# Kernel tuning notes

Measured on AMD Instinct MI355X. Metric: run time of the kernel, lower is better.

## Reference

```python
import jax, jax.numpy as jnp
import numpy as np

B, N, T = 512, 128, 64
ALPHA = 0.5  # LeakyReLU negative slope
NEG = jnp.float32(-9e15)


def _gat(h, mask, W, a):
    # GraphAttentionLayer with concat=True (trailing relu), eval mode (no dropout)
    Wh = h @ W                                   # [B,N,F]
    F = W.shape[1]
    e1 = Wh @ a[:F]                              # [B,N,1]
    e2 = Wh @ a[F:]                              # [B,N,1]
    e = jax.nn.leaky_relu(e1 + jnp.swapaxes(e2, 1, 2), ALPHA)  # [B,N,N]
    e = jnp.where(mask, e, NEG)
    att = jax.nn.softmax(e, axis=1)              # torch softmax dim=1 (over rows)
    return jax.nn.relu(jnp.matmul(att, Wh))


def _lstm_layer(x, wih, whh, bih, bhh):
    # x: [T,B,in]; hidden size 1; torch gate order i,f,g,o
    h0 = jnp.zeros((x.shape[1], 1), x.dtype)
    def step(carry, xt):
        h, c = carry
        g = xt @ wih.T + h @ whh.T + bih + bhh   # [B,4]
        i, f, gg, o = jnp.split(g, 4, axis=-1)
        c = jax.nn.sigmoid(f) * c + jax.nn.sigmoid(i) * jnp.tanh(gg)
        h = jax.nn.sigmoid(o) * jnp.tanh(c)
        return (h, c), h
    _, ys = jax.lax.scan(step, (h0, h0), x)
    return ys                                    # [T,B,1]


def setup_inputs() -> dict:
    key = jax.random.key(0)
    ks = jax.random.split(key, 32)
    def xu(k, shape, gain=1.414):
        lim = gain * np.sqrt(6.0 / (shape[0] + shape[1]))
        return jax.random.uniform(k, shape, jnp.float32, -lim, lim)
    d = {}
    d["adjacency"] = jax.random.randint(ks[0], (B, N, N), 0, 2, dtype=jnp.int32)
    d["feature"] = jax.random.normal(ks[1], (B, N), jnp.float32)
    d["time"] = jax.random.normal(ks[2], (B, N), jnp.float32)
    d["interval_popularity"] = jax.random.normal(ks[3], (B, T), jnp.float32)
    # GAT params
    d["W1"] = xu(ks[4], (1, 512)); d["a1"] = xu(ks[5], (1024, 1))
    d["W2"] = xu(ks[6], (512, 8)); d["a2"] = xu(ks[7], (16, 1))
    # attention-pooling params (torch.randn in original)
    d["Weight"] = jax.random.normal(ks[8], (128, 128), jnp.float32)
    d["Wv"] = jax.random.normal(ks[9], (128, 128), jnp.float32)
    # 2-layer LSTM(1->1)
    d["wih0"] = jax.random.normal(ks[10], (4, 1)) * 0.5
    d["whh0"] = jax.random.normal(ks[11], (4, 1)) * 0.5
    d["bih0"] = jax.random.normal(ks[12], (4,)) * 0.5
    d["bhh0"] = jax.random.normal(ks[13], (4,)) * 0.5
    d["wih1"] = jax.random.normal(ks[14], (4, 1)) * 0.5
    d["whh1"] = jax.random.normal(ks[15], (4, 1)) * 0.5
    d["bih1"] = jax.random.normal(ks[16], (4,)) * 0.5
    d["bhh1"] = jax.random.normal(ks[17], (4,)) * 0.5
    # MultiheadAttention(embed_dim=1, heads=1)
    d["mha_in_w"] = jax.random.normal(ks[18], (3, 1)) * 0.5
    d["mha_in_b"] = jnp.zeros((3,), jnp.float32)
    d["mha_out_w"] = jax.random.normal(ks[19], (1, 1)) * 0.5
    d["mha_out_b"] = jnp.zeros((1,), jnp.float32)
    # FL MLP: 192->128->32->1 (stored as [in,out])
    d["fl1_w"] = xu(ks[20], (192, 128), 1.0); d["fl1_b"] = jnp.zeros((128,), jnp.float32)
    d["fl2_w"] = xu(ks[21], (128, 32), 1.0);  d["fl2_b"] = jnp.zeros((32,), jnp.float32)
    d["fl3_w"] = xu(ks[22], (32, 1), 1.0);    d["fl3_b"] = jnp.zeros((1,), jnp.float32)
    return d


def reference(adjacency, feature, time, interval_popularity,
              W1, a1, W2, a2, Weight, Wv,
              wih0, whh0, bih0, bhh0, wih1, whh1, bih1, bhh1,
              mha_in_w, mha_in_b, mha_out_w, mha_out_b,
              fl1_w, fl1_b, fl2_w, fl2_b, fl3_w, fl3_b):
    mask = adjacency > 0
    x = feature.reshape(B, N, -1)                # [B,128,1]
    h = _gat(x, mask, W1, a1)                    # [B,128,512]
    h = jax.nn.relu(h)
    h = _gat(h, mask, W2, a2)                    # [B,128,8]

    xs = jnp.swapaxes(interval_popularity.reshape(B, -1, 1), 0, 1)  # [T,B,1]
    xs = _lstm_layer(xs, wih0, whh0, bih0, bhh0)
    xs = _lstm_layer(xs, wih1, whh1, bih1, bhh1)
    ip = jnp.swapaxes(xs, 0, 1).reshape(B, -1)   # [B,64]

    h = jnp.mean(h, axis=2, keepdims=True)       # [B,128,1]
    Wt = time.reshape(B, N, -1)                  # [B,128,1]
    att = jnp.concatenate([h, Wt], axis=2)       # [B,128,2]
    att = jnp.swapaxes(jnp.swapaxes(att, 1, 2) @ Weight, 1, 2)  # [B,128,2]
    att = jax.nn.softmax(att, axis=2)
    hv = jnp.swapaxes(jnp.concatenate([h, Wt], axis=2), 1, 2)   # [B,2,128]
    hv = jax.nn.relu((hv @ Wv).reshape(B, N, -1))  # faithful reshape (not transpose)
    h = jnp.sum(hv * att, axis=2)                # [B,128]

    h = jnp.concatenate([h, ip], axis=1)         # [B,192]
    hq = h[..., None]                            # [B,192,1]
    q = hq * mha_in_w[0, 0] + mha_in_b[0]
    k = hq * mha_in_w[1, 0] + mha_in_b[1]
    v = hq * mha_in_w[2, 0] + mha_in_b[2]
    a = jax.nn.softmax(q @ jnp.swapaxes(k, 1, 2), axis=-1)  # scale=1/sqrt(1)
    ho = (a @ v) * mha_out_w[0, 0] + mha_out_b[0]
    h = (ho + hq).reshape(B, -1)                 # [B,192]

    h = jax.nn.relu(h @ fl1_w + fl1_b)
    h = jnp.tanh(h @ fl2_w + fl2_b)
    h = jax.nn.relu(h @ fl3_w + fl3_b)           # [B,1]
    return h
```

## Files before the change

kernel.cpp:

```cpp
#include <hip/hip_runtime.h>
#include <math.h>

typedef unsigned int uint;
typedef unsigned long long ull;

#define L2E 1.44269504f

__device__ __forceinline__ float lrelu(float z){ return fmaxf(z, 0.5f*z); }
__device__ __forceinline__ float reluf(float z){ return fmaxf(z, 0.f); }
__device__ __forceinline__ float fexp(float z){ return __builtin_amdgcn_exp2f(z*L2E); }
__device__ __forceinline__ float frcp(float z){ return __builtin_amdgcn_rcpf(z); }
__device__ __forceinline__ float tanh_n(float z){
  return __fmaf_rn(2.f, __builtin_amdgcn_rcpf(1.f + __builtin_amdgcn_exp2f(-2.f*L2E*z)), -1.f);
}

__global__ __launch_bounds__(512, 4) void fused_kernel(
    const int* __restrict__ adj, const float* __restrict__ feat,
    const float* __restrict__ timei,
    const float* __restrict__ Weight, const float* __restrict__ Wv,
    const float* __restrict__ W1, const float* __restrict__ a1,
    const float* __restrict__ W2, const float* __restrict__ a2,
    const float* __restrict__ ipop,
    const float* __restrict__ wih0, const float* __restrict__ whh0,
    const float* __restrict__ bih0, const float* __restrict__ bhh0,
    const float* __restrict__ wih1, const float* __restrict__ whh1,
    const float* __restrict__ bih1, const float* __restrict__ bhh1,
    const float* __restrict__ mha_in_w, const float* __restrict__ mha_in_b,
    const float* __restrict__ mha_out_w, const float* __restrict__ mha_out_b,
    const float* __restrict__ fl1_w, const float* __restrict__ fl1_b,
    const float* __restrict__ fl2_w, const float* __restrict__ fl2_b,
    const float* __restrict__ fl3_w, const float* __restrict__ fl3_b,
    float* __restrict__ out)
{
  const int b = blockIdx.x, t = threadIdx.x;
  const int lane = t & 127, h = t >> 7;
  const int wv = t >> 6, ln = t & 63;

  __shared__ ull   rowW[256];
  __shared__ float xs[128], tim[128], hm[128], eAs[128], rho_s[128];
  __shared__ float2 f2a[128];
  __shared__ float  red1[4][128];
  __shared__ float2 red4[4][128];
  __shared__ float4 q4[128];
  __shared__ float4 pool4[4][128];
  __shared__ float2 kv[192];
  __shared__ float  hq[192], h2s[192];
  __shared__ float  pden[2][192], pnum[2][192];
  __shared__ float  sred[8];
  __shared__ float  cpart[8][2];
  __shared__ float  pqpart[8][16];
  __shared__ float  cons[24];
  __shared__ float  ips[64];

  if (t < 128){ xs[t] = feat[b*128 + t]; tim[t] = timei[b*128 + t]; }

  float a2reg[16];
  if (t == 0){
    #pragma unroll
    for (int g = 0; g < 16; ++g) a2reg[g] = a2[g];
  }

  float h1v=0.f, c1s=0.f, h2v=0.f, c2s=0.f;
  float wi0s[4], wh0s[4], bb0s[4], wi1s[4], wh1s[4], bb1s[4];
  const float4* xsrc4 = (const float4*)(ipop + b*64);
  float4 xcur0, xcur1;
  if (t == 511){
    #pragma unroll
    for (int k = 0; k < 4; ++k){
      const float s = (k == 2) ? -2.f*L2E : -L2E;
      wi0s[k]=wih0[k]*s; wh0s[k]=whh0[k]*s; bb0s[k]=(bih0[k]+bhh0[k])*s;
      wi1s[k]=wih1[k]*s; wh1s[k]=whh1[k]*s; bb1s[k]=(bih1[k]+bhh1[k])*s;
    }
    xcur0 = xsrc4[0]; xcur1 = xsrc4[1];
  }
  auto lstm8 = [&](int c){
    if (t != 511) return;
    const float4 xa = xcur0, xb = xcur1;
    if (c < 7){ xcur0 = xsrc4[2*c+2]; xcur1 = xsrc4[2*c+3]; }
    float o[8];
    #pragma unroll
    for (int si = 0; si < 8; ++si){
      const float x = (si==0)?xa.x:(si==1)?xa.y:(si==2)?xa.z:(si==3)?xa.w:
                      (si==4)?xb.x:(si==5)?xb.y:(si==6)?xb.z:xb.w;
      float gi = frcp(1.f + __builtin_amdgcn_exp2f(__fmaf_rn(x, wi0s[0], __fmaf_rn(h1v, wh0s[0], bb0s[0]))));
      float gf = frcp(1.f + __builtin_amdgcn_exp2f(__fmaf_rn(x, wi0s[1], __fmaf_rn(h1v, wh0s[1], bb0s[1]))));
      float gg = __fmaf_rn(2.f, frcp(1.f + __builtin_amdgcn_exp2f(__fmaf_rn(x, wi0s[2], __fmaf_rn(h1v, wh0s[2], bb0s[2])))), -1.f);
      float go = frcp(1.f + __builtin_amdgcn_exp2f(__fmaf_rn(x, wi0s[3], __fmaf_rn(h1v, wh0s[3], bb0s[3]))));
      c1s = gf*c1s + gi*gg;  h1v = go*tanh_n(c1s);
      float hi = frcp(1.f + __builtin_amdgcn_exp2f(__fmaf_rn(h1v, wi1s[0], __fmaf_rn(h2v, wh1s[0], bb1s[0]))));
      float hf = frcp(1.f + __builtin_amdgcn_exp2f(__fmaf_rn(h1v, wi1s[1], __fmaf_rn(h2v, wh1s[1], bb1s[1]))));
      float hg = __fmaf_rn(2.f, frcp(1.f + __builtin_amdgcn_exp2f(__fmaf_rn(h1v, wi1s[2], __fmaf_rn(h2v, wh1s[2], bb1s[2])))), -1.f);
      float ho = frcp(1.f + __builtin_amdgcn_exp2f(__fmaf_rn(h1v, wi1s[3], __fmaf_rn(h2v, wh1s[3], bb1s[3])))) ;
      c2s = hf*c2s + hi*hg;  h2v = ho*tanh_n(c2s);
      o[si] = h2v;
    }
    #pragma unroll
    for (int si = 0; si < 8; ++si) ips[8*c + si] = o[si];
  };

  {
    const int* abase = adj + (((long)b) << 14) + wv*2048 + ln;
    ull myword = 0;
    #pragma unroll
    for (int blk = 0; blk < 4; ++blk){
      int v[8];
      #pragma unroll
      for (int q = 0; q < 8; ++q) v[q] = abase[(blk*8 + q)*64];
      #pragma unroll
      for (int q = 0; q < 8; ++q){
        ull m = __ballot(v[q] > 0);
        myword = (ln == blk*8 + q) ? m : myword;
      }
    }
    if (ln < 32) rowW[wv*32 + ln] = myword;
  }

  {
    float w0 = W1[t];
    float s1 = w0*a1[t];
    float s2 = w0*a1[512+t];
    #pragma unroll
    for (int off = 32; off; off >>= 1){ s1 += __shfl_xor(s1, off); s2 += __shfl_xor(s2, off); }
    if (ln == 0){ cpart[wv][0] = s1; cpart[wv][1] = s2; }
  }
  {
    const float w = W1[t];
    const float wp = fmaxf(w, 0.f), wn = fminf(w, 0.f);
    const float4 A = *(const float4*)(W2 + t*8);
    const float4 Bv = *(const float4*)(W2 + t*8 + 4);
    float accP[8], accQ[8];
    accP[0]=wp*A.x;  accQ[0]=wn*A.x;   accP[1]=wp*A.y;  accQ[1]=wn*A.y;
    accP[2]=wp*A.z;  accQ[2]=wn*A.z;   accP[3]=wp*A.w;  accQ[3]=wn*A.w;
    accP[4]=wp*Bv.x; accQ[4]=wn*Bv.x;  accP[5]=wp*Bv.y; accQ[5]=wn*Bv.y;
    accP[6]=wp*Bv.z; accQ[6]=wn*Bv.z;  accP[7]=wp*Bv.w; accQ[7]=wn*Bv.w;
    #pragma unroll
    for (int g = 0; g < 8; ++g){
      float p = accP[g], q = accQ[g];
      #pragma unroll
      for (int off = 32; off; off >>= 1){ p += __shfl_xor(p, off); q += __shfl_xor(q, off); }
      if (ln == 0){ pqpart[wv][g] = p; pqpart[wv][8+g] = q; }
    }
  }
  __syncthreads();

  const uint rowm = (uint)(rowW[lane*2 + (h>>1)] >> ((h&1)*32));
  uint colm = 0;
  {
    const int wsel = lane >> 6, bsel = lane & 63;
    #pragma unroll
    for (int k = 0; k < 32; ++k)
      colm |= (uint)((rowW[(32*h + k)*2 + wsel] >> bsel) & 1ull) << k;
  }
  if (t < 64){
    float mx = fmaxf(xs[t], xs[t+64]);
    float mn = fminf(xs[t], xs[t+64]);
    #pragma unroll
    for (int off = 32; off; off >>= 1){
      mx = fmaxf(mx, __shfl_xor(mx, off));
      mn = fminf(mn, __shfl_xor(mn, off));
    }
    if (t == 0){ sred[0] = mx; sred[1] = mn; }
  }
  if (t == 0){
    float c1v = 0.f, c2v = 0.f;
    #pragma unroll
    for (int wvi = 0; wvi < 8; ++wvi){ c1v += cpart[wvi][0]; c2v += cpart[wvi][1]; }
    cons[0] = c1v; cons[1] = c2v;
    float pAx=0.f, qAx=0.f, pBx=0.f, qBx=0.f;
    #pragma unroll
    for (int g = 0; g < 8; ++g){
      float P = 0.f, Q = 0.f;
      #pragma unroll
      for (int wvi = 0; wvi < 8; ++wvi){ P += pqpart[wvi][g]; Q += pqpart[wvi][8+g]; }
      cons[2+g] = P; cons[10+g] = Q;
      pAx = __fmaf_rn(P, a2reg[g],   pAx);  qAx = __fmaf_rn(Q, a2reg[g],   qAx);
      pBx = __fmaf_rn(P, a2reg[8+g], pBx);  qBx = __fmaf_rn(Q, a2reg[8+g], qBx);
    }
    cons[18]=pAx; cons[19]=qAx; cons[20]=pBx; cons[21]=qBx;
  }
  lstm8(0);
  __syncthreads();

  float myE1=0.f, myRho=0.f, myx=0.f;
  {
    const float c1 = cons[0], c2 = cons[1];
    const float rmax = (c1 >= 0.f) ? c1*sred[0] : c1*sred[1];
    if (t < 128){
      myx = xs[t];
      float r  = c1*myx;
      float cj = c2*myx;
      float d  = r - rmax;
      myE1 = fexp(d);
      float Eh = fexp(0.5f*d);
      myRho = fexp(-0.5f*fmaxf(rmax + cj, -170.f));
      f2a[t] = make_float2(myE1, Eh);
      rho_s[t] = myRho;
    }
  }
  lstm8(1);
  __syncthreads();

  {
    const float rho = rho_s[lane];
    float s = 0.f;
    #pragma unroll
    for (int k = 0; k < 32; ++k){
      float2 E = f2a[32*h + k];
      float v = fmaxf(E.x, rho*E.y);
      s += ((colm >> k) & 1u) ? v : 0.f;
    }
    red1[h][lane] = s;
  }
  lstm8(2);
  __syncthreads();

  if (t < 128){
    float s = red1[0][t] + red1[1][t] + red1[2][t] + red1[3][t];
    float sinv = frcp(s);
    float ax = fabsf(myx)*sinv;
    q4[t] = make_float4(ax, myRho*ax, (myx >= 0.f) ? 1.f : -1.f, 0.f);
  }
  lstm8(3);
  __syncthreads();

  {
    const float om = frcp(f2a[lane].y);
    float acc = 0.f;
    #pragma unroll
    for (int k = 0; k < 32; ++k){
      float4 G = q4[32*h + k];
      float v = fmaxf(G.x, om*G.y);
      float sg = ((rowm >> k) & 1u) ? G.z : 0.f;
      acc = __fmaf_rn(v, sg, acc);
    }
    red1[h][lane] = acc;
  }
  lstm8(4);
  __syncthreads();

  float u = 0.f, eBv = 0.f, eAv = 0.f;
  if (t < 128){
    u = myE1*(red1[0][t] + red1[1][t] + red1[2][t] + red1[3][t]);
    eAv = (u >= 0.f ? cons[18] : cons[19])*u;
    eBv = (u >= 0.f ? cons[20] : cons[21])*u;
    eAs[t] = eAv;
  }
  lstm8(5);
  __syncthreads();

  if (t < 64){
    float mx = fmaxf(eAs[t], eAs[t+64]);
    #pragma unroll
    for (int off = 32; off; off >>= 1) mx = fmaxf(mx, __shfl_xor(mx, off));
    if (t == 0) sred[2] = mx;
  }
  lstm8(6);
  __syncthreads();

  float myE1b=0.f;
  {
    const float eAmax = sred[2];
    if (t < 128){
      float d2 = eAv - eAmax;
      myE1b = fexp(d2);
      float Ehb = fexp(0.5f*d2);
      float rho2 = fexp(-0.5f*fmaxf(eAmax + eBv, -170.f));
      f2a[t] = make_float2(myE1b, Ehb);
      rho_s[t] = rho2;
    }
  }
  lstm8(7);
  __syncthreads();

  {
    const float rho = rho_s[lane];
    float s = 0.f;
    #pragma unroll
    for (int k = 0; k < 32; ++k){
      float2 E = f2a[32*h + k];
      float v = fmaxf(E.x, rho*E.y);
      s += ((colm >> k) & 1u) ? v : 0.f;
    }
    red1[h][lane] = s;
  }
  __syncthreads();

  if (t < 128){
    float s = red1[0][t] + red1[1][t] + red1[2][t] + red1[3][t];
    float sinv = frcp(s);
    float rho2 = rho_s[t];
    float up = fmaxf(u, 0.f)*sinv, un = -fminf(u, 0.f)*sinv;
    q4[t] = make_float4(up, rho2*up, un, rho2*un);
  }
  __syncthreads();

  {
    const float om = frcp(f2a[lane].y);
    float accp = 0.f, accn = 0.f;
    #pragma unroll
    for (int k = 0; k < 32; ++k){
      float4 G = q4[32*h + k];
      bool m = ((rowm >> k) & 1u);
      float v1 = fmaxf(G.x, om*G.y);
      float v2 = fmaxf(G.z, om*G.w);
      accp += m ? v1 : 0.f;
      accn += m ? v2 : 0.f;
    }
    red4[h][lane] = make_float2(accp, accn);
  }
  __syncthreads();

  if (t < 128){
    float ap=0.f, an=0.f;
    #pragma unroll
    for (int g = 0; g < 4; ++g){ float2 v = red4[g][t]; ap += v.x; an += v.y; }
    float sp = myE1b*ap, sn = -myE1b*an;
    float acc = 0.f;
    #pragma unroll
    for (int g = 0; g < 8; ++g) acc += reluf(__fmaf_rn(sp, cons[2+g], sn*cons[10+g]));
    hm[t] = 0.125f*acc;
  }
  __syncthreads();

  {
    const int n = lane;
    float a0=0.f, a1v=0.f, v0=0.f, v1=0.f;
    const int m0 = h*32;
    #pragma unroll 8
    for (int k = 0; k < 32; ++k){
      int m = m0 + k;
      float hmv = hm[m], tv = tim[m];
      float wg = Weight[(m<<7) + n], wvv = Wv[(m<<7) + n];
      a0 = __fmaf_rn(hmv, wg, a0); a1v = __fmaf_rn(tv, wg, a1v);
      v0 = __fmaf_rn(hmv, wvv, v0); v1 = __fmaf_rn(tv, wvv, v1);
    }
    pool4[h][n] = make_float4(a0, a1v, v0, v1);
  }
  __syncthreads();

  float att0 = 0.f, att1 = 0.f, rsv = 0.f;
  if (t < 128){
    float A0=0.f, A1=0.f, V0=0.f, V1=0.f;
    #pragma unroll
    for (int g = 0; g < 4; ++g){ float4 v = pool4[g][t]; A0+=v.x; A1+=v.y; V0+=v.z; V1+=v.w; }
    red4[0][t] = make_float2(V0, V1);
    float mx = fmaxf(A0, A1);
    att0 = fexp(A0 - mx); att1 = fexp(A1 - mx);
    rsv = frcp(att0 + att1);
  }
  __syncthreads();

  if (t < 128){
    float r0, r1;
    if (t < 64){ r0 = red4[0][2*t].x;     r1 = red4[0][2*t+1].x; }
    else       { r0 = red4[0][2*t-128].y; r1 = red4[0][2*t-127].y; }
    hq[t] = (reluf(r0)*att0 + reluf(r1)*att1)*rsv;
  }
  if (t >= 192 && t < 256) hq[128 + (t - 192)] = ips[t - 192];
  __syncthreads();

  const float wq = mha_in_w[0], wk = mha_in_w[1], wvv_ = mha_in_w[2];
  const float bq = mha_in_b[0], bk = mha_in_b[1], bv = mha_in_b[2];
  const float wo = mha_out_w[0], bo = mha_out_b[0];
  if (t < 192){
    float hv_ = hq[t];
    kv[t] = make_float2(__fmaf_rn(hv_, wk, bk), __fmaf_rn(hv_, wvv_, bv));
  }
  __syncthreads();

  if (t < 64){
    float k0 = kv[t].x, k1 = kv[t+64].x, k2 = kv[t+128].x;
    float mx = fmaxf(fmaxf(k0, k1), k2);
    float mn = fminf(fminf(k0, k1), k2);
    #pragma unroll
    for (int off = 32; off; off >>= 1){
      mx = fmaxf(mx, __shfl_xor(mx, off));
      mn = fminf(mn, __shfl_xor(mn, off));
    }
    if (t == 0){ sred[3] = mx; sred[4] = mn; }
  }
  __syncthreads();

  if (t < 384){
    const int half = (t >= 192), tt = t - half*192;
    float qi = __fmaf_rn(hq[tt], wq, bq);
    float mx = (qi >= 0.f) ? qi*sred[3] : qi*sred[4];
    const float qi2 = qi*L2E, mx2 = mx*L2E;
    float den = 0.f, num = 0.f;
    const int j0 = half*96;
    #pragma unroll 8
    for (int jj = 0; jj < 96; ++jj){
      float2 K = kv[j0 + jj];
      float e = __builtin_amdgcn_exp2f(__fmaf_rn(qi2, K.x, -mx2));
      den += e; num = __fmaf_rn(e, K.y, num);
    }
    pden[half][tt] = den; pnum[half][tt] = num;
  }
  __syncthreads();

  if (t < 192){
    float den = pden[0][t] + pden[1][t];
    float num = pnum[0][t] + pnum[1][t];
    h2s[t] = __fmaf_rn(num*frcp(den), wo, bo) + hq[t];
  }
  __syncthreads();

  {
    const int n = t & 127, qtr = t >> 7;
    float acc = 0.f;
    const int i0 = qtr*48;
    #pragma unroll 8
    for (int k = 0; k < 48; ++k){
      int i = i0 + k;
      acc = __fmaf_rn(h2s[i], fl1_w[i*128 + n], acc);
    }
    red4[qtr][n].x = acc;
  }
  __syncthreads();

  if (t < 128) rho_s[t] = reluf(red4[0][t].x + red4[1][t].x + red4[2][t].x + red4[3][t].x + fl1_b[t]);
  __syncthreads();

  if (t < 128){
    const int n = t & 31, seg = t >> 5;
    float p = 0.f;
    #pragma unroll 8
    for (int k = 0; k < 32; ++k){
      int i = seg*32 + k;
      p = __fmaf_rn(rho_s[i], fl2_w[i*32 + n], p);
    }
    eAs[t] = p;
  }
  __syncthreads();

  if (t < 32) hm[t] = tanh_n(eAs[t] + eAs[t+32] + eAs[t+64] + eAs[t+96] + fl2_b[t]);
  __syncthreads();

  if (t < 64){
    float p = (t < 32) ? hm[t]*fl3_w[t] : 0.f;
    #pragma unroll
    for (int off = 32; off; off >>= 1) p += __shfl_xor(p, off);
    if (t == 0) out[b] = reluf(p + fl3_b[0]);
  }
}

extern "C" void kernel_launch(void* const* d_in, const int* in_sizes, int n_in,
                              void* d_out, int out_size, void* d_ws, size_t ws_size,
                              hipStream_t stream) {
  const int*   adj    = (const int*)  d_in[0];
  const float* feat   = (const float*)d_in[1];
  const float* timei  = (const float*)d_in[2];
  const float* ipop   = (const float*)d_in[3];
  const float* W1     = (const float*)d_in[4];
  const float* a1     = (const float*)d_in[5];
  const float* W2     = (const float*)d_in[6];
  const float* a2     = (const float*)d_in[7];
  const float* Weight = (const float*)d_in[8];
  const float* Wv     = (const float*)d_in[9];
  const float* wih0   = (const float*)d_in[10];
  const float* whh0   = (const float*)d_in[11];
  const float* bih0   = (const float*)d_in[12];
  const float* bhh0   = (const float*)d_in[13];
  const float* wih1   = (const float*)d_in[14];
  const float* whh1   = (const float*)d_in[15];
  const float* bih1   = (const float*)d_in[16];
  const float* bhh1   = (const float*)d_in[17];
  const float* mha_in_w  = (const float*)d_in[18];
  const float* mha_in_b  = (const float*)d_in[19];
  const float* mha_out_w = (const float*)d_in[20];
  const float* mha_out_b = (const float*)d_in[21];
  const float* fl1_w = (const float*)d_in[22];
  const float* fl1_b = (const float*)d_in[23];
  const float* fl2_w = (const float*)d_in[24];
  const float* fl2_b = (const float*)d_in[25];
  const float* fl3_w = (const float*)d_in[26];
  const float* fl3_b = (const float*)d_in[27];

  fused_kernel<<<512, 512, 0, stream>>>(adj, feat, timei, Weight, Wv,
                                        W1, a1, W2, a2, ipop,
                                        wih0, whh0, bih0, bhh0,
                                        wih1, whh1, bih1, bhh1,
                                        mha_in_w, mha_in_b, mha_out_w, mha_out_b,
                                        fl1_w, fl1_b, fl2_w, fl2_b, fl3_w, fl3_b,
                                        (float*)d_out);
}
```

Baseline: 49.29 us.

## Double block size to 1024 threads and halve per-thread work in every stage

Each block now runs 1024 threads instead of 512, and every stage is re-split so each thread does half as many items: adjacency ballots, GAT column sums, pooling, MHA key ranges and the FC layers. Reduction buffers grow to 8 partial slots. The goal is to cut the serial per-thread loop length and add wavefronts for latency hiding, given only 512 blocks. The cost is more partial-sum reduction, more register pressure under the tighter launch bound, and more threads sitting idle in the narrow stages.

```diff
diff --git a/kernel.cpp b/kernel.cpp
--- a/kernel.cpp
+++ b/kernel.cpp
@@ -6,7 +6,6 @@
 
 #define L2E 1.44269504f
 
-__device__ __forceinline__ float lrelu(float z){ return fmaxf(z, 0.5f*z); }
 __device__ __forceinline__ float reluf(float z){ return fmaxf(z, 0.f); }
 __device__ __forceinline__ float fexp(float z){ return __builtin_amdgcn_exp2f(z*L2E); }
 __device__ __forceinline__ float frcp(float z){ return __builtin_amdgcn_rcpf(z); }
@@ -14,7 +13,7 @@
   return __fmaf_rn(2.f, __builtin_amdgcn_rcpf(1.f + __builtin_amdgcn_exp2f(-2.f*L2E*z)), -1.f);
 }
 
-__global__ __launch_bounds__(512, 4) void fused_kernel(
+__global__ __launch_bounds__(1024, 8) void fused_kernel(
     const int* __restrict__ adj, const float* __restrict__ feat,
     const float* __restrict__ timei,
     const float* __restrict__ Weight, const float* __restrict__ Wv,
@@ -39,13 +38,13 @@
   __shared__ ull   rowW[256];
   __shared__ float xs[128], tim[128], hm[128], eAs[128], rho_s[128];
   __shared__ float2 f2a[128];
-  __shared__ float  red1[4][128];
-  __shared__ float2 red4[4][128];
+  __shared__ float  red1[8][128];
+  __shared__ float2 red2f[8][128];
   __shared__ float4 q4[128];
-  __shared__ float4 pool4[4][128];
+  __shared__ float4 pool4[8][128];
   __shared__ float2 kv[192];
   __shared__ float  hq[192], h2s[192];
-  __shared__ float  pden[2][192], pnum[2][192];
+  __shared__ float  pden[4][192], pnum[4][192];
   __shared__ float  sred[8];
   __shared__ float  cpart[8][2];
   __shared__ float  pqpart[8][16];
@@ -64,7 +63,7 @@
   float wi0s[4], wh0s[4], bb0s[4], wi1s[4], wh1s[4], bb1s[4];
   const float4* xsrc4 = (const float4*)(ipop + b*64);
   float4 xcur0, xcur1;
-  if (t == 511){
+  if (t == 1023){
     #pragma unroll
     for (int k = 0; k < 4; ++k){
       const float s = (k == 2) ? -2.f*L2E : -L2E;
@@ -74,7 +73,7 @@
     xcur0 = xsrc4[0]; xcur1 = xsrc4[1];
   }
   auto lstm8 = [&](int c){
-    if (t != 511) return;
+    if (t != 1023) return;
     const float4 xa = xcur0, xb = xcur1;
     if (c < 7){ xcur0 = xsrc4[2*c+2]; xcur1 = xsrc4[2*c+3]; }
     float o[8];
@@ -99,10 +98,10 @@
   };
 
   {
-    const int* abase = adj + (((long)b) << 14) + wv*2048 + ln;
+    const int* abase = adj + (((long)b) << 14) + wv*1024 + ln;
     ull myword = 0;
     #pragma unroll
-    for (int blk = 0; blk < 4; ++blk){
+    for (int blk = 0; blk < 2; ++blk){
       int v[8];
       #pragma unroll
       for (int q = 0; q < 8; ++q) v[q] = abase[(blk*8 + q)*64];
@@ -112,19 +111,17 @@
         myword = (ln == blk*8 + q) ? m : myword;
       }
     }
-    if (ln < 32) rowW[wv*32 + ln] = myword;
-  }
-
-  {
+    if (ln < 16) rowW[wv*16 + ln] = myword;
+  }
+
+  if (t < 512){
     float w0 = W1[t];
     float s1 = w0*a1[t];
     float s2 = w0*a1[512+t];
     #pragma unroll
     for (int off = 32; off; off >>= 1){ s1 += __shfl_xor(s1, off); s2 += __shfl_xor(s2, off); }
     if (ln == 0){ cpart[wv][0] = s1; cpart[wv][1] = s2; }
-  }
-  {
-    const float w = W1[t];
+    const float w = w0;
     const float wp = fmaxf(w, 0.f), wn = fminf(w, 0.f);
     const float4 A = *(const float4*)(W2 + t*8);
     const float4 Bv = *(const float4*)(W2 + t*8 + 4);
@@ -143,13 +140,13 @@
   }
   __syncthreads();
 
-  const uint rowm = (uint)(rowW[lane*2 + (h>>1)] >> ((h&1)*32));
+  const uint rowm = (uint)((rowW[lane*2 + (h>>2)] >> ((h&3)*16)) & 0xFFFFull);
   uint colm = 0;
   {
     const int wsel = lane >> 6, bsel = lane & 63;
-    #pragma unroll
-    for (int k = 0; k < 32; ++k)
-      colm |= (uint)((rowW[(32*h + k)*2 + wsel] >> bsel) & 1ull) << k;
+    #pragma unroll 8
+    for (int k = 0; k < 16; ++k)
+      colm |= (uint)((rowW[(16*h + k)*2 + wsel] >> bsel) & 1ull) << k;
   }
   if (t < 64){
     float mx = fmaxf(xs[t], xs[t+64]);
@@ -203,9 +200,9 @@
   {
     const float rho = rho_s[lane];
     float s = 0.f;
-    #pragma unroll
-    for (int k = 0; k < 32; ++k){
-      float2 E = f2a[32*h + k];
+    #pragma unroll 8
+    for (int k = 0; k < 16; ++k){
+      float2 E = f2a[16*h + k];
       float v = fmaxf(E.x, rho*E.y);
       s += ((colm >> k) & 1u) ? v : 0.f;
     }
@@ -215,7 +212,9 @@
   __syncthreads();
 
   if (t < 128){
-    float s = red1[0][t] + red1[1][t] + red1[2][t] + red1[3][t];
+    float s = 0.f;
+    #pragma unroll
+    for (int g = 0; g < 8; ++g) s += red1[g][t];
     float sinv = frcp(s);
     float ax = fabsf(myx)*sinv;
     q4[t] = make_float4(ax, myRho*ax, (myx >= 0.f) ? 1.f : -1.f, 0.f);
@@ -226,9 +225,9 @@
   {
     const float om = frcp(f2a[lane].y);
     float acc = 0.f;
-    #pragma unroll
-    for (int k = 0; k < 32; ++k){
-      float4 G = q4[32*h + k];
+    #pragma unroll 8
+    for (int k = 0; k < 16; ++k){
+      float4 G = q4[16*h + k];
       float v = fmaxf(G.x, om*G.y);
       float sg = ((rowm >> k) & 1u) ? G.z : 0.f;
       acc = __fmaf_rn(v, sg, acc);
@@ -240,7 +239,10 @@
 
   float u = 0.f, eBv = 0.f, eAv = 0.f;
   if (t < 128){
-    u = myE1*(red1[0][t] + red1[1][t] + red1[2][t] + red1[3][t]);
+    float s = 0.f;
+    #pragma unroll
+    for (int g = 0; g < 8; ++g) s += red1[g][t];
+    u = myE1*s;
     eAv = (u >= 0.f ? cons[18] : cons[19])*u;
     eBv = (u >= 0.f ? cons[20] : cons[21])*u;
     eAs[t] = eAv;
@@ -275,9 +277,9 @@
   {
     const float rho = rho_s[lane];
     float s = 0.f;
-    #pragma unroll
-    for (int k = 0; k < 32; ++k){
-      float2 E = f2a[32*h + k];
+    #pragma unroll 8
+    for (int k = 0; k < 16; ++k){
+      float2 E = f2a[16*h + k];
       float v = fmaxf(E.x, rho*E.y);
       s += ((colm >> k) & 1u) ? v : 0.f;
     }
@@ -286,7 +288,9 @@
   __syncthreads();
 
   if (t < 128){
-    float s = red1[0][t] + red1[1][t] + red1[2][t] + red1[3][t];
+    float s = 0.f;
+    #pragma unroll
+    for (int g = 0; g < 8; ++g) s += red1[g][t];
     float sinv = frcp(s);
     float rho2 = rho_s[t];
     float up = fmaxf(u, 0.f)*sinv, un = -fminf(u, 0.f)*sinv;
@@ -297,23 +301,23 @@
   {
     const float om = frcp(f2a[lane].y);
     float accp = 0.f, accn = 0.f;
-    #pragma unroll
-    for (int k = 0; k < 32; ++k){
-      float4 G = q4[32*h + k];
+    #pragma unroll 8
+    for (int k = 0; k < 16; ++k){
+      float4 G = q4[16*h + k];
       bool m = ((rowm >> k) & 1u);
       float v1 = fmaxf(G.x, om*G.y);
       float v2 = fmaxf(G.z, om*G.w);
       accp += m ? v1 : 0.f;
       accn += m ? v2 : 0.f;
     }
-    red4[h][lane] = make_float2(accp, accn);
+    red2f[h][lane] = make_float2(accp, accn);
   }
   __syncthreads();
 
   if (t < 128){
     float ap=0.f, an=0.f;
     #pragma unroll
-    for (int g = 0; g < 4; ++g){ float2 v = red4[g][t]; ap += v.x; an += v.y; }
+    for (int g = 0; g < 8; ++g){ float2 v = red2f[g][t]; ap += v.x; an += v.y; }
     float sp = myE1b*ap, sn = -myE1b*an;
     float acc = 0.f;
     #pragma unroll
@@ -325,9 +329,9 @@
   {
     const int n = lane;
     float a0=0.f, a1v=0.f, v0=0.f, v1=0.f;
-    const int m0 = h*32;
-    #pragma unroll 8
-    for (int k = 0; k < 32; ++k){
+    const int m0 = h*16;
+    #pragma unroll 8
+    for (int k = 0; k < 16; ++k){
       int m = m0 + k;
       float hmv = hm[m], tv = tim[m];
       float wg = Weight[(m<<7) + n], wvv = Wv[(m<<7) + n];
@@ -342,8 +346,8 @@
   if (t < 128){
     float A0=0.f, A1=0.f, V0=0.f, V1=0.f;
     #pragma unroll
-    for (int g = 0; g < 4; ++g){ float4 v = pool4[g][t]; A0+=v.x; A1+=v.y; V0+=v.z; V1+=v.w; }
-    red4[0][t] = make_float2(V0, V1);
+    for (int g = 0; g < 8; ++g){ float4 v = pool4[g][t]; A0+=v.x; A1+=v.y; V0+=v.z; V1+=v.w; }
+    red2f[0][t] = make_float2(V0, V1);
     float mx = fmaxf(A0, A1);
     att0 = fexp(A0 - mx); att1 = fexp(A1 - mx);
     rsv = frcp(att0 + att1);
@@ -352,8 +356,8 @@
 
   if (t < 128){
     float r0, r1;
-    if (t < 64){ r0 = red4[0][2*t].x;     r1 = red4[0][2*t+1].x; }
-    else       { r0 = red4[0][2*t-128].y; r1 = red4[0][2*t-127].y; }
+    if (t < 64){ r0 = red2f[0][2*t].x;     r1 = red2f[0][2*t+1].x; }
+    else       { r0 = red2f[0][2*t-128].y; r1 = red2f[0][2*t-127].y; }
     hq[t] = (reluf(r0)*att0 + reluf(r1)*att1)*rsv;
   }
   if (t >= 192 && t < 256) hq[128 + (t - 192)] = ips[t - 192];
@@ -381,59 +385,69 @@
   }
   __syncthreads();
 
-  if (t < 384){
-    const int half = (t >= 192), tt = t - half*192;
+  if (t < 768){
+    const int qtr = t / 192, tt = t - qtr*192;
     float qi = __fmaf_rn(hq[tt], wq, bq);
     float mx = (qi >= 0.f) ? qi*sred[3] : qi*sred[4];
     const float qi2 = qi*L2E, mx2 = mx*L2E;
     float den = 0.f, num = 0.f;
-    const int j0 = half*96;
-    #pragma unroll 8
-    for (int jj = 0; jj < 96; ++jj){
+    const int j0 = qtr*48;
+    #pragma unroll 8
+    for (int jj = 0; jj < 48; ++jj){
       float2 K = kv[j0 + jj];
       float e = __builtin_amdgcn_exp2f(__fmaf_rn(qi2, K.x, -mx2));
       den += e; num = __fmaf_rn(e, K.y, num);
     }
-    pden[half][tt] = den; pnum[half][tt] = num;
+    pden[qtr][tt] = den; pnum[qtr][tt] = num;
   }
   __syncthreads();
 
   if (t < 192){
-    float den = pden[0][t] + pden[1][t];
-    float num = pnum[0][t] + pnum[1][t];
+    float den = pden[0][t] + pden[1][t] + pden[2][t] + pden[3][t];
+    float num = pnum[0][t] + pnum[1][t] + pnum[2][t] + pnum[3][t];
     h2s[t] = __fmaf_rn(num*frcp(den), wo, bo) + hq[t];
   }
   __syncthreads();
 
   {
-    const int n = t & 127, qtr = t >> 7;
+    const int n = t & 127, oct = t >> 7;
     float acc = 0.f;
-    const int i0 = qtr*48;
-    #pragma unroll 8
-    for (int k = 0; k < 48; ++k){
+    const int i0 = oct*24;
+    #pragma unroll 8
+    for (int k = 0; k < 24; ++k){
       int i = i0 + k;
       acc = __fmaf_rn(h2s[i], fl1_w[i*128 + n], acc);
     }
-    red4[qtr][n].x = acc;
-  }
-  __syncthreads();
-
-  if (t < 128) rho_s[t] = reluf(red4[0][t].x + red4[1][t].x + red4[2][t].x + red4[3][t].x + fl1_b[t]);
-  __syncthreads();
-
-  if (t < 128){
+    red1[oct][n] = acc;
+  }
+  __syncthreads();
+
+  if (t < 128){
+    float s = fl1_b[t];
+    #pragma unroll
+    for (int g = 0; g < 8; ++g) s += red1[g][t];
+    rho_s[t] = reluf(s);
+  }
+  __syncthreads();
+
+  if (t < 256){
     const int n = t & 31, seg = t >> 5;
     float p = 0.f;
     #pragma unroll 8
-    for (int k = 0; k < 32; ++k){
-      int i = seg*32 + k;
+    for (int k = 0; k < 16; ++k){
+      int i = seg*16 + k;
       p = __fmaf_rn(rho_s[i], fl2_w[i*32 + n], p);
     }
-    eAs[t] = p;
-  }
-  __syncthreads();
-
-  if (t < 32) hm[t] = tanh_n(eAs[t] + eAs[t+32] + eAs[t+64] + eAs[t+96] + fl2_b[t]);
+    red1[seg][n] = p;
+  }
+  __syncthreads();
+
+  if (t < 32){
+    float s = fl2_b[t];
+    #pragma unroll
+    for (int g = 0; g < 8; ++g) s += red1[g][t];
+    hm[t] = tanh_n(s);
+  }
   __syncthreads();
 
   if (t < 64){
@@ -476,11 +490,11 @@
   const float* fl3_w = (const float*)d_in[26];
   const float* fl3_b = (const float*)d_in[27];
 
-  fused_kernel<<<512, 512, 0, stream>>>(adj, feat, timei, Weight, Wv,
-                                        W1, a1, W2, a2, ipop,
-                                        wih0, whh0, bih0, bhh0,
-                                        wih1, whh1, bih1, bhh1,
-                                        mha_in_w, mha_in_b, mha_out_w, mha_out_b,
-                                        fl1_w, fl1_b, fl2_w, fl2_b, fl3_w, fl3_b,
-                                        (float*)d_out);
+  fused_kernel<<<512, 1024, 0, stream>>>(adj, feat, timei, Weight, Wv,
+                                         W1, a1, W2, a2, ipop,
+                                         wih0, whh0, bih0, bhh0,
+                                         wih1, whh1, bih1, bhh1,
+                                         mha_in_w, mha_in_b, mha_out_w, mha_out_b,
+                                         fl1_w, fl1_b, fl2_w, fl2_b, fl3_w, fl3_b,
+                                         (float*)d_out);
 }
```

After: 49.69 us. Within noise of the previous version (+0.8%).

## Cut block barriers by recomputing reductions per wavefront and fusing phases

Applied to the files above, without the earlier changes.

Each wavefront now computes the max/min reductions redundantly instead of having one wave write them to shared memory behind an extra barrier. The per-node normalisation (sum of partials, reciprocal) moves into the consumer loops, which removes the intermediate q4 stage and its barriers. The small tail phases (fl2 reduce plus tanh) are fused, and the LSTM steps are spread over the remaining barriers. The price is redundant arithmetic and shared-memory reads in the inner loops, and the launch-bounds occupancy hint is dropped.

```diff
diff --git a/kernel.cpp b/kernel.cpp
--- a/kernel.cpp
+++ b/kernel.cpp
@@ -6,7 +6,6 @@
 
 #define L2E 1.44269504f
 
-__device__ __forceinline__ float lrelu(float z){ return fmaxf(z, 0.5f*z); }
 __device__ __forceinline__ float reluf(float z){ return fmaxf(z, 0.f); }
 __device__ __forceinline__ float fexp(float z){ return __builtin_amdgcn_exp2f(z*L2E); }
 __device__ __forceinline__ float frcp(float z){ return __builtin_amdgcn_rcpf(z); }
@@ -14,7 +13,7 @@
   return __fmaf_rn(2.f, __builtin_amdgcn_rcpf(1.f + __builtin_amdgcn_exp2f(-2.f*L2E*z)), -1.f);
 }
 
-__global__ __launch_bounds__(512, 4) void fused_kernel(
+__global__ __launch_bounds__(512) void fused_kernel(
     const int* __restrict__ adj, const float* __restrict__ feat,
     const float* __restrict__ timei,
     const float* __restrict__ Weight, const float* __restrict__ Wv,
@@ -37,16 +36,14 @@
   const int wv = t >> 6, ln = t & 63;
 
   __shared__ ull   rowW[256];
-  __shared__ float xs[128], tim[128], hm[128], eAs[128], rho_s[128];
+  __shared__ float xs[128], tim[128], hm[128], eAs[128], rho_s[128], us[128];
   __shared__ float2 f2a[128];
   __shared__ float  red1[4][128];
-  __shared__ float2 red4[4][128];
-  __shared__ float4 q4[128];
+  __shared__ float2 red2f[4][128];
   __shared__ float4 pool4[4][128];
   __shared__ float2 kv[192];
   __shared__ float  hq[192], h2s[192];
   __shared__ float  pden[2][192], pnum[2][192];
-  __shared__ float  sred[8];
   __shared__ float  cpart[8][2];
   __shared__ float  pqpart[8][16];
   __shared__ float  cons[24];
@@ -151,21 +148,36 @@
     for (int k = 0; k < 32; ++k)
       colm |= (uint)((rowW[(32*h + k)*2 + wsel] >> bsel) & 1ull) << k;
   }
-  if (t < 64){
-    float mx = fmaxf(xs[t], xs[t+64]);
-    float mn = fminf(xs[t], xs[t+64]);
+  float c1r = 0.f, c2r = 0.f;
+  #pragma unroll
+  for (int wvi = 0; wvi < 8; ++wvi){ c1r += cpart[wvi][0]; c2r += cpart[wvi][1]; }
+  float wmx, wmn;
+  {
+    float mx = fmaxf(xs[ln], xs[ln+64]);
+    float mn = fminf(xs[ln], xs[ln+64]);
     #pragma unroll
     for (int off = 32; off; off >>= 1){
       mx = fmaxf(mx, __shfl_xor(mx, off));
       mn = fminf(mn, __shfl_xor(mn, off));
     }
-    if (t == 0){ sred[0] = mx; sred[1] = mn; }
+    wmx = mx; wmn = mn;
+  }
+  float myE1=0.f, myRho=0.f, myx=0.f;
+  {
+    const float rmax = (c1r >= 0.f) ? c1r*wmx : c1r*wmn;
+    if (t < 128){
+      myx = xs[t];
+      float r  = c1r*myx;
+      float cj = c2r*myx;
+      float d  = r - rmax;
+      myE1 = fexp(d);
+      float Eh = fexp(0.5f*d);
+      myRho = fexp(-0.5f*fmaxf(rmax + cj, -170.f));
+      f2a[t] = make_float2(myE1, Eh);
+      rho_s[t] = myRho;
+    }
   }
   if (t == 0){
-    float c1v = 0.f, c2v = 0.f;
-    #pragma unroll
-    for (int wvi = 0; wvi < 8; ++wvi){ c1v += cpart[wvi][0]; c2v += cpart[wvi][1]; }
-    cons[0] = c1v; cons[1] = c2v;
     float pAx=0.f, qAx=0.f, pBx=0.f, qBx=0.f;
     #pragma unroll
     for (int g = 0; g < 8; ++g){
@@ -181,25 +193,6 @@
   lstm8(0);
   __syncthreads();
 
-  float myE1=0.f, myRho=0.f, myx=0.f;
-  {
-    const float c1 = cons[0], c2 = cons[1];
-    const float rmax = (c1 >= 0.f) ? c1*sred[0] : c1*sred[1];
-    if (t < 128){
-      myx = xs[t];
-      float r  = c1*myx;
-      float cj = c2*myx;
-      float d  = r - rmax;
-      myE1 = fexp(d);
-      float Eh = fexp(0.5f*d);
-      myRho = fexp(-0.5f*fmaxf(rmax + cj, -170.f));
-      f2a[t] = make_float2(myE1, Eh);
-      rho_s[t] = myRho;
-    }
-  }
-  lstm8(1);
-  __syncthreads();
-
   {
     const float rho = rho_s[lane];
     float s = 0.f;
@@ -211,55 +204,45 @@
     }
     red1[h][lane] = s;
   }
-  lstm8(2);
-  __syncthreads();
-
-  if (t < 128){
-    float s = red1[0][t] + red1[1][t] + red1[2][t] + red1[3][t];
-    float sinv = frcp(s);
-    float ax = fabsf(myx)*sinv;
-    q4[t] = make_float4(ax, myRho*ax, (myx >= 0.f) ? 1.f : -1.f, 0.f);
-  }
-  lstm8(3);
+  lstm8(1);
   __syncthreads();
 
   {
     const float om = frcp(f2a[lane].y);
     float acc = 0.f;
-    #pragma unroll
-    for (int k = 0; k < 32; ++k){
-      float4 G = q4[32*h + k];
-      float v = fmaxf(G.x, om*G.y);
-      float sg = ((rowm >> k) & 1u) ? G.z : 0.f;
+    #pragma unroll 8
+    for (int k = 0; k < 32; ++k){
+      int j = 32*h + k;
+      float s = red1[0][j] + red1[1][j] + red1[2][j] + red1[3][j];
+      float sinv = frcp(s);
+      float xj = xs[j];
+      float ax = fabsf(xj)*sinv;
+      float v = fmaxf(ax, om*(rho_s[j]*ax));
+      float sg = ((rowm >> k) & 1u) ? ((xj >= 0.f) ? 1.f : -1.f) : 0.f;
       acc = __fmaf_rn(v, sg, acc);
     }
-    red1[h][lane] = acc;
-  }
-  lstm8(4);
+    red2f[h][lane].x = acc;
+  }
+  lstm8(2);
   __syncthreads();
 
   float u = 0.f, eBv = 0.f, eAv = 0.f;
   if (t < 128){
-    u = myE1*(red1[0][t] + red1[1][t] + red1[2][t] + red1[3][t]);
+    u = myE1*(red2f[0][t].x + red2f[1][t].x + red2f[2][t].x + red2f[3][t].x);
     eAv = (u >= 0.f ? cons[18] : cons[19])*u;
     eBv = (u >= 0.f ? cons[20] : cons[21])*u;
     eAs[t] = eAv;
-  }
-  lstm8(5);
-  __syncthreads();
-
-  if (t < 64){
-    float mx = fmaxf(eAs[t], eAs[t+64]);
+    us[t] = u;
+  }
+  lstm8(3);
+  __syncthreads();
+
+  float myE1b=0.f;
+  {
+    float mx = fmaxf(eAs[ln], eAs[ln+64]);
     #pragma unroll
     for (int off = 32; off; off >>= 1) mx = fmaxf(mx, __shfl_xor(mx, off));
-    if (t == 0) sred[2] = mx;
-  }
-  lstm8(6);
-  __syncthreads();
-
-  float myE1b=0.f;
-  {
-    const float eAmax = sred[2];
+    const float eAmax = mx;
     if (t < 128){
       float d2 = eAv - eAmax;
       myE1b = fexp(d2);
@@ -269,7 +252,7 @@
       rho_s[t] = rho2;
     }
   }
-  lstm8(7);
+  lstm8(4);
   __syncthreads();
 
   {
@@ -283,43 +266,42 @@
     }
     red1[h][lane] = s;
   }
-  __syncthreads();
-
-  if (t < 128){
-    float s = red1[0][t] + red1[1][t] + red1[2][t] + red1[3][t];
-    float sinv = frcp(s);
-    float rho2 = rho_s[t];
-    float up = fmaxf(u, 0.f)*sinv, un = -fminf(u, 0.f)*sinv;
-    q4[t] = make_float4(up, rho2*up, un, rho2*un);
-  }
+  lstm8(5);
   __syncthreads();
 
   {
     const float om = frcp(f2a[lane].y);
     float accp = 0.f, accn = 0.f;
-    #pragma unroll
-    for (int k = 0; k < 32; ++k){
-      float4 G = q4[32*h + k];
+    #pragma unroll 8
+    for (int k = 0; k < 32; ++k){
+      int j = 32*h + k;
+      float s = red1[0][j] + red1[1][j] + red1[2][j] + red1[3][j];
+      float sinv = frcp(s);
+      float uj = us[j];
+      float rho2j = rho_s[j];
+      float up = fmaxf(uj, 0.f)*sinv, un = -fminf(uj, 0.f)*sinv;
+      float v1 = fmaxf(up, om*(rho2j*up));
+      float v2 = fmaxf(un, om*(rho2j*un));
       bool m = ((rowm >> k) & 1u);
-      float v1 = fmaxf(G.x, om*G.y);
-      float v2 = fmaxf(G.z, om*G.w);
       accp += m ? v1 : 0.f;
       accn += m ? v2 : 0.f;
     }
-    red4[h][lane] = make_float2(accp, accn);
-  }
+    red2f[h][lane] = make_float2(accp, accn);
+  }
+  lstm8(6);
   __syncthreads();
 
   if (t < 128){
     float ap=0.f, an=0.f;
     #pragma unroll
-    for (int g = 0; g < 4; ++g){ float2 v = red4[g][t]; ap += v.x; an += v.y; }
+    for (int g = 0; g < 4; ++g){ float2 v = red2f[g][t]; ap += v.x; an += v.y; }
     float sp = myE1b*ap, sn = -myE1b*an;
     float acc = 0.f;
     #pragma unroll
     for (int g = 0; g < 8; ++g) acc += reluf(__fmaf_rn(sp, cons[2+g], sn*cons[10+g]));
     hm[t] = 0.125f*acc;
   }
+  lstm8(7);
   __syncthreads();
 
   {
@@ -343,7 +325,7 @@
     float A0=0.f, A1=0.f, V0=0.f, V1=0.f;
     #pragma unroll
     for (int g = 0; g < 4; ++g){ float4 v = pool4[g][t]; A0+=v.x; A1+=v.y; V0+=v.z; V1+=v.w; }
-    red4[0][t] = make_float2(V0, V1);
+    red2f[0][t] = make_float2(V0, V1);
     float mx = fmaxf(A0, A1);
     att0 = fexp(A0 - mx); att1 = fexp(A1 - mx);
     rsv = frcp(att0 + att1);
@@ -352,8 +334,8 @@
 
   if (t < 128){
     float r0, r1;
-    if (t < 64){ r0 = red4[0][2*t].x;     r1 = red4[0][2*t+1].x; }
-    else       { r0 = red4[0][2*t-128].y; r1 = red4[0][2*t-127].y; }
+    if (t < 64){ r0 = red2f[0][2*t].x;     r1 = red2f[0][2*t+1].x; }
+    else       { r0 = red2f[0][2*t-128].y; r1 = red2f[0][2*t-127].y; }
     hq[t] = (reluf(r0)*att0 + reluf(r1)*att1)*rsv;
   }
   if (t >= 192 && t < 256) hq[128 + (t - 192)] = ips[t - 192];
@@ -368,8 +350,8 @@
   }
   __syncthreads();
 
-  if (t < 64){
-    float k0 = kv[t].x, k1 = kv[t+64].x, k2 = kv[t+128].x;
+  {
+    float k0 = kv[ln].x, k1 = kv[ln+64].x, k2 = kv[ln+128].x;
     float mx = fmaxf(fmaxf(k0, k1), k2);
     float mn = fminf(fminf(k0, k1), k2);
     #pragma unroll
@@ -377,24 +359,21 @@
       mx = fmaxf(mx, __shfl_xor(mx, off));
       mn = fminf(mn, __shfl_xor(mn, off));
     }
-    if (t == 0){ sred[3] = mx; sred[4] = mn; }
-  }
-  __syncthreads();
-
-  if (t < 384){
-    const int half = (t >= 192), tt = t - half*192;
-    float qi = __fmaf_rn(hq[tt], wq, bq);
-    float mx = (qi >= 0.f) ? qi*sred[3] : qi*sred[4];
-    const float qi2 = qi*L2E, mx2 = mx*L2E;
-    float den = 0.f, num = 0.f;
-    const int j0 = half*96;
-    #pragma unroll 8
-    for (int jj = 0; jj < 96; ++jj){
-      float2 K = kv[j0 + jj];
-      float e = __builtin_amdgcn_exp2f(__fmaf_rn(qi2, K.x, -mx2));
-      den += e; num = __fmaf_rn(e, K.y, num);
-    }
-    pden[half][tt] = den; pnum[half][tt] = num;
+    if (t < 384){
+      const int half = (t >= 192), tt = t - half*192;
+      float qi = __fmaf_rn(hq[tt], wq, bq);
+      float mxx = (qi >= 0.f) ? qi*mx : qi*mn;
+      const float qi2 = qi*L2E, mx2 = mxx*L2E;
+      float den = 0.f, num = 0.f;
+      const int j0 = half*96;
+      #pragma unroll 8
+      for (int jj = 0; jj < 96; ++jj){
+        float2 K = kv[j0 + jj];
+        float e = __builtin_amdgcn_exp2f(__fmaf_rn(qi2, K.x, -mx2));
+        den += e; num = __fmaf_rn(e, K.y, num);
+      }
+      pden[half][tt] = den; pnum[half][tt] = num;
+    }
   }
   __syncthreads();
 
@@ -414,11 +393,11 @@
       int i = i0 + k;
       acc = __fmaf_rn(h2s[i], fl1_w[i*128 + n], acc);
     }
-    red4[qtr][n].x = acc;
-  }
-  __syncthreads();
-
-  if (t < 128) rho_s[t] = reluf(red4[0][t].x + red4[1][t].x + red4[2][t].x + red4[3][t].x + fl1_b[t]);
+    red1[qtr][n] = acc;
+  }
+  __syncthreads();
+
+  if (t < 128) rho_s[t] = reluf(red1[0][t] + red1[1][t] + red1[2][t] + red1[3][t] + fl1_b[t]);
   __syncthreads();
 
   if (t < 128){
@@ -429,15 +408,16 @@
       int i = seg*32 + k;
       p = __fmaf_rn(rho_s[i], fl2_w[i*32 + n], p);
     }
-    eAs[t] = p;
-  }
-  __syncthreads();
-
-  if (t < 32) hm[t] = tanh_n(eAs[t] + eAs[t+32] + eAs[t+64] + eAs[t+96] + fl2_b[t]);
+    red1[seg][n] = p;
+  }
   __syncthreads();
 
   if (t < 64){
-    float p = (t < 32) ? hm[t]*fl3_w[t] : 0.f;
+    float p = 0.f;
+    if (t < 32){
+      float s = red1[0][t] + red1[1][t] + red1[2][t] + red1[3][t] + fl2_b[t];
+      p = tanh_n(s)*fl3_w[t];
+    }
     #pragma unroll
     for (int off = 32; off; off >>= 1) p += __shfl_xor(p, off);
     if (t == 0) out[b] = reluf(p + fl3_b[0]);
```

Measured after the change: 65.02 us. +31.9%, slower.
